# Kernel optimization log

Measured on AMD Instinct MI355X. Metric: run time of the kernel, lower is better.

## Reference

```python
import jax, jax.numpy as jnp
import numpy as np

N_NODES = 2_000_000  # divisible by 5 for the final view(-1, 5)
N_EDGES = 32_000_000


def setup_inputs() -> dict:
    key = jax.random.key(0)
    k_x, k_e, k_w, k_b, k_w1, k_b1, k_w2, k_b2 = jax.random.split(key, 8)
    x = jax.random.normal(k_x, (N_NODES, 1), dtype=jnp.float32)
    edge_index = jax.random.randint(k_e, (2, N_EDGES), 0, N_NODES, dtype=jnp.int64)
    # GCNConv(1, 1): linear weight [in=1, out=1] (no bias in lin), separate bias [1]
    w_conv = jax.random.normal(k_w, (1, 1), dtype=jnp.float32)
    b_conv = jax.random.normal(k_b, (1,), dtype=jnp.float32) * 0.1
    # MLP: Linear(2,4) -> ReLU -> Linear(4,1); weights stored as [in, out]
    w1 = jax.random.normal(k_w1, (2, 4), dtype=jnp.float32) * 0.5
    b1 = jax.random.normal(k_b1, (4,), dtype=jnp.float32) * 0.1
    w2 = jax.random.normal(k_w2, (4, 1), dtype=jnp.float32) * 0.5
    b2 = jax.random.normal(k_b2, (1,), dtype=jnp.float32) * 0.1
    return {"x": x, "edge_index": edge_index, "w_conv": w_conv, "b_conv": b_conv,
            "w1": w1, "b1": b1, "w2": w2, "b2": b2}


def reference(x, edge_index, w_conv, b_conv, w1, b1, w2, b2):
    # GCNConv with normalize=False: no self-loops, no degree norm.
    # h = x @ W; out[dst] = sum over incoming edges of h[src]; out += bias
    src, dst = edge_index[0], edge_index[1]
    h = x @ w_conv                                   # [N, 1]
    agg = jax.ops.segment_sum(h[src], dst, num_segments=N_NODES) + b_conv  # [N, 1]
    # intermediate MLP on cat([x_prev, x_prev], dim=1)
    z = jnp.concatenate([agg, agg], axis=1)          # [N, 2]
    z = jnp.maximum(z @ w1 + b1, 0.0) @ w2 + b2      # [N, 1]
    return z.reshape(-1, 5)[:, 0]                    # [N/5]
```

## Files before the change

kernel.cpp:

```cpp
#include <hip/hip_runtime.h>

#define N_NODES 2000000
#define N_EDGES 32000000
#define N_OUT   400000
#define NBUCKET 256
#define BSZ     1568
#define CAP_BLK 64
#define CHUNK   32768
#define CAP_BKT 28672
#define KSLICE  4

typedef int iv4 __attribute__((ext_vector_type(4)));

__global__ __launch_bounds__(256, 2) void p1_bin(
    const int* __restrict__ src,
    const int* __restrict__ dst,
    const float* __restrict__ x,
    unsigned* __restrict__ cnt,
    float* __restrict__ partials,
    unsigned* __restrict__ payload)
{
    __shared__ unsigned s_cur[NBUCKET];
    __shared__ unsigned s_base[NBUCKET];
    __shared__ unsigned s_stage[NBUCKET][CAP_BLK];

    const int tid = threadIdx.x;
    if (tid < NBUCKET) s_cur[tid] = 0;
    __syncthreads();

    const long long blockStart = (long long)blockIdx.x * CHUNK;
    const int NIT = CHUNK / 1024;

    long long b0 = blockStart + (long long)tid * 4;
    bool valid0 = (b0 < N_EDGES);
    iv4 d4 = valid0 ? *reinterpret_cast<const iv4*>(dst + b0) : (iv4)0;
    iv4 s4 = valid0 ? *reinterpret_cast<const iv4*>(src + b0) : (iv4)0;

    for (int it = 0; it < NIT; ++it) {
        iv4 nd = (iv4)0, ns = (iv4)0;
        bool nvalid = false;
        if (it + 1 < NIT) {
            const long long bn = blockStart + (long long)(it + 1) * 1024 + tid * 4;
            nvalid = (bn < N_EDGES);
            if (nvalid) {
                nd = *reinterpret_cast<const iv4*>(dst + bn);
                ns = *reinterpret_cast<const iv4*>(src + bn);
            }
        }
        if (valid0) {
#pragma unroll
            for (int j = 0; j < 4; ++j) {
                const int d = d4[j];
                if (d % 5 == 0) {
                    const int g = d / 5;
                    const int b = g / BSZ;
                    const unsigned local = (unsigned)(g - b * BSZ);
                    const unsigned p = ((unsigned)s4[j] << 11) | local;
                    const unsigned slot = atomicAdd(&s_cur[b], 1u);
                    if (slot < CAP_BLK) {
                        s_stage[b][slot] = p;
                    } else {
                        const float v = x[s4[j]];
                        atomicAdd(&partials[((size_t)b * (KSLICE + 1) + KSLICE) * BSZ + local], v);
                    }
                }
            }
        }
        d4 = nd; s4 = ns; valid0 = nvalid;
    }
    __syncthreads();

    if (tid < NBUCKET) {
        const unsigned c = min(s_cur[tid], (unsigned)CAP_BLK);
        s_cur[tid] = c;
        s_base[tid] = atomicAdd(&cnt[tid], c);
    }
    __syncthreads();

    const int wave = tid >> 6, lane = tid & 63;
    for (int b = wave; b < NBUCKET; b += 4) {
        const unsigned c = s_cur[b];
        if ((unsigned)lane < c)
            payload[(size_t)b * CAP_BKT + s_base[b] + lane] = s_stage[b][lane];
    }
}

__global__ __launch_bounds__(256) void p2_accum(
    const unsigned* __restrict__ cnt,
    const unsigned* __restrict__ payload,
    const float* __restrict__ x,
    float* __restrict__ partials)
{
    __shared__ float acc[BSZ];
    const int b = blockIdx.x >> 2;
    const int j = blockIdx.x & 3;
    const int tid = threadIdx.x;

    for (int i = tid; i < BSZ; i += 256) acc[i] = 0.0f;
    __syncthreads();

    unsigned n = cnt[b];
    if (n > CAP_BKT) n = CAP_BKT;
    const unsigned beg = (unsigned)(((unsigned long long)n * j) / KSLICE);
    const unsigned end = (unsigned)(((unsigned long long)n * (j + 1)) / KSLICE);
    const unsigned* pb = payload + (size_t)b * CAP_BKT;

    unsigned i0 = beg + tid;
    for (; i0 + 7u * 256u < end; i0 += 8u * 256u) {
        unsigned pv[8]; float vv[8];
#pragma unroll
        for (int u = 0; u < 8; ++u) pv[u] = pb[i0 + u * 256u];
#pragma unroll
        for (int u = 0; u < 8; ++u) vv[u] = x[pv[u] >> 11];
#pragma unroll
        for (int u = 0; u < 8; ++u)
            __hip_atomic_fetch_add(&acc[pv[u] & 2047u], vv[u],
                                   __ATOMIC_RELAXED, __HIP_MEMORY_SCOPE_WORKGROUP);
    }
    for (; i0 < end; i0 += 256u) {
        const unsigned p = pb[i0];
        const float v = x[p >> 11];
        __hip_atomic_fetch_add(&acc[p & 2047u], v,
                               __ATOMIC_RELAXED, __HIP_MEMORY_SCOPE_WORKGROUP);
    }
    __syncthreads();

    float* row = partials + ((size_t)b * (KSLICE + 1) + j) * BSZ;
    for (int i = tid; i < BSZ; i += 256) row[i] = acc[i];
}

__global__ __launch_bounds__(256) void p3_out(
    const float* __restrict__ partials,
    const float* __restrict__ w_conv,
    const float* __restrict__ b_conv,
    const float* __restrict__ w1,
    const float* __restrict__ b1,
    const float* __restrict__ w2,
    const float* __restrict__ b2,
    float* __restrict__ out)
{
    const int i = blockIdx.x * 256 + threadIdx.x;
    if (i >= N_OUT) return;
    const int b = i / BSZ;
    const int local = i - b * BSZ;
    const float* pr = partials + (size_t)b * (KSLICE + 1) * BSZ + local;
    float s = 0.0f;
#pragma unroll
    for (int r = 0; r <= KSLICE; ++r) s += pr[(size_t)r * BSZ];
    const float a = s * w_conv[0] + b_conv[0];
    float rr = b2[0];
#pragma unroll
    for (int jj = 0; jj < 4; ++jj) {
        float t = fmaf(a, w1[jj] + w1[4 + jj], b1[jj]);
        rr = fmaf(fmaxf(t, 0.0f), w2[jj], rr);
    }
    out[i] = rr;
}

__global__ __launch_bounds__(256, 4) void gcn_edge_scatter_dev(
    const int* __restrict__ src,
    const int* __restrict__ dst,
    const float* __restrict__ x,
    float* __restrict__ agg)
{
    const long long base = ((long long)blockIdx.x * blockDim.x + threadIdx.x) * 16;
    if (base >= N_EDGES) return;
    iv4 d4[4], s4[4];
#pragma unroll
    for (int c = 0; c < 4; ++c)
        d4[c] = *(reinterpret_cast<const iv4*>(dst + base) + c);
#pragma unroll
    for (int c = 0; c < 4; ++c)
        s4[c] = *(reinterpret_cast<const iv4*>(src + base) + c);
    int dd[16]; int idx[16]; bool pass[16];
#pragma unroll
    for (int c = 0; c < 4; ++c)
#pragma unroll
        for (int j = 0; j < 4; ++j) {
            const int d = d4[c][j];
            const bool p = (d % 5 == 0);
            dd[c * 4 + j] = d; pass[c * 4 + j] = p;
            idx[c * 4 + j] = p ? s4[c][j] : 0;
        }
    float v[16];
#pragma unroll
    for (int k = 0; k < 16; ++k) v[k] = x[idx[k]];
#pragma unroll
    for (int k = 0; k < 16; ++k)
        if (pass[k]) atomicAdd(&agg[dd[k] / 5], v[k]);
}

__global__ __launch_bounds__(256) void gcn_epilogue_fb(
    const float* __restrict__ agg,
    const float* __restrict__ w_conv, const float* __restrict__ b_conv,
    const float* __restrict__ w1, const float* __restrict__ b1,
    const float* __restrict__ w2, const float* __restrict__ b2,
    float* __restrict__ out)
{
    const int i = blockIdx.x * 256 + threadIdx.x;
    if (i >= N_OUT) return;
    const float a = agg[i] * w_conv[0] + b_conv[0];
    float r = b2[0];
#pragma unroll
    for (int j = 0; j < 4; ++j) {
        float t = fmaf(a, w1[j] + w1[4 + j], b1[j]);
        r = fmaf(fmaxf(t, 0.0f), w2[j], r);
    }
    out[i] = r;
}

extern "C" void kernel_launch(void* const* d_in, const int* in_sizes, int n_in,
                              void* d_out, int out_size, void* d_ws, size_t ws_size,
                              hipStream_t stream) {
    const float* x      = (const float*)d_in[0];
    const int*   ei     = (const int*)  d_in[1];
    const float* w_conv = (const float*)d_in[2];
    const float* b_conv = (const float*)d_in[3];
    const float* w1     = (const float*)d_in[4];
    const float* b1     = (const float*)d_in[5];
    const float* w2     = (const float*)d_in[6];
    const float* b2     = (const float*)d_in[7];
    float* out = (float*)d_out;

    const size_t part_off   = 1024;
    const size_t part_bytes = (size_t)NBUCKET * (KSLICE + 1) * BSZ * sizeof(float);
    const size_t pay_off    = (part_off + part_bytes + 255) & ~(size_t)255;
    const size_t pay_bytes  = (size_t)NBUCKET * CAP_BKT * sizeof(unsigned);
    const size_t need       = pay_off + pay_bytes;

    if (ws_size >= need) {
        unsigned* cnt      = (unsigned*)d_ws;
        float*    partials = (float*)((char*)d_ws + part_off);
        unsigned* payload  = (unsigned*)((char*)d_ws + pay_off);

        (void)hipMemsetAsync(d_ws, 0, pay_off, stream);

        const int grid_p1 = (int)((N_EDGES + CHUNK - 1) / CHUNK);
        p1_bin<<<grid_p1, 256, 0, stream>>>(ei, ei + N_EDGES, x, cnt, partials, payload);
        p2_accum<<<NBUCKET * KSLICE, 256, 0, stream>>>(cnt, payload, x, partials);
        p3_out<<<(N_OUT + 255) / 256, 256, 0, stream>>>(
            partials, w_conv, b_conv, w1, b1, w2, b2, out);
    } else {
        float* agg = (float*)d_ws;
        (void)hipMemsetAsync(agg, 0, (size_t)N_OUT * sizeof(float), stream);
        gcn_edge_scatter_dev<<<(N_EDGES / 16 + 255) / 256, 256, 0, stream>>>(
            ei, ei + N_EDGES, x, agg);
        gcn_epilogue_fb<<<(N_OUT + 255) / 256, 256, 0, stream>>>(
            agg, w_conv, b_conv, w1, b1, w2, b2, out);
    }
}
```

Baseline: 457.0 us.

## Shrink binning chunk, split overflow buffer, vectorize accumulation and raise occupancy

Halves the per-block edge chunk and staging capacity so p1 uses less LDS and can run four blocks per CU, and uses nontemporal loads for the streamed edge arrays. Moves overflow accumulation into its own buffer so only counters and overflow need zeroing, shrinking the memset. Pads bucket counters to separate cache lines, and rewrites the p1 writeback to cover two buckets per wave. p2 now uses 512-thread blocks with 4-wide payload loads. Smaller staging raises the chance of spills into the global atomic overflow path.

```diff
diff --git a/kernel.cpp b/kernel.cpp
--- a/kernel.cpp
+++ b/kernel.cpp
@@ -5,19 +5,21 @@
 #define N_OUT   400000
 #define NBUCKET 256
 #define BSZ     1568
-#define CAP_BLK 64
-#define CHUNK   32768
+#define CAP_BLK 32
+#define CHUNK   16384
 #define CAP_BKT 28672
 #define KSLICE  4
+#define CNT_STRIDE 16
 
 typedef int iv4 __attribute__((ext_vector_type(4)));
-
-__global__ __launch_bounds__(256, 2) void p1_bin(
+typedef unsigned uv4 __attribute__((ext_vector_type(4)));
+
+__global__ __launch_bounds__(256, 4) void p1_bin(
     const int* __restrict__ src,
     const int* __restrict__ dst,
     const float* __restrict__ x,
     unsigned* __restrict__ cnt,
-    float* __restrict__ partials,
+    float* __restrict__ overflow,
     unsigned* __restrict__ payload)
 {
     __shared__ unsigned s_cur[NBUCKET];
@@ -33,8 +35,8 @@
 
     long long b0 = blockStart + (long long)tid * 4;
     bool valid0 = (b0 < N_EDGES);
-    iv4 d4 = valid0 ? *reinterpret_cast<const iv4*>(dst + b0) : (iv4)0;
-    iv4 s4 = valid0 ? *reinterpret_cast<const iv4*>(src + b0) : (iv4)0;
+    iv4 d4 = valid0 ? __builtin_nontemporal_load(reinterpret_cast<const iv4*>(dst + b0)) : (iv4)0;
+    iv4 s4 = valid0 ? __builtin_nontemporal_load(reinterpret_cast<const iv4*>(src + b0)) : (iv4)0;
 
     for (int it = 0; it < NIT; ++it) {
         iv4 nd = (iv4)0, ns = (iv4)0;
@@ -43,25 +45,25 @@
             const long long bn = blockStart + (long long)(it + 1) * 1024 + tid * 4;
             nvalid = (bn < N_EDGES);
             if (nvalid) {
-                nd = *reinterpret_cast<const iv4*>(dst + bn);
-                ns = *reinterpret_cast<const iv4*>(src + bn);
+                nd = __builtin_nontemporal_load(reinterpret_cast<const iv4*>(dst + bn));
+                ns = __builtin_nontemporal_load(reinterpret_cast<const iv4*>(src + bn));
             }
         }
         if (valid0) {
 #pragma unroll
             for (int j = 0; j < 4; ++j) {
-                const int d = d4[j];
-                if (d % 5 == 0) {
-                    const int g = d / 5;
-                    const int b = g / BSZ;
-                    const unsigned local = (unsigned)(g - b * BSZ);
+                const unsigned d = (unsigned)d4[j];
+                if (d % 5u == 0u) {
+                    const unsigned g = d / 5u;
+                    const unsigned b = g / (unsigned)BSZ;
+                    const unsigned local = g - b * (unsigned)BSZ;
                     const unsigned p = ((unsigned)s4[j] << 11) | local;
                     const unsigned slot = atomicAdd(&s_cur[b], 1u);
                     if (slot < CAP_BLK) {
                         s_stage[b][slot] = p;
                     } else {
                         const float v = x[s4[j]];
-                        atomicAdd(&partials[((size_t)b * (KSLICE + 1) + KSLICE) * BSZ + local], v);
+                        atomicAdd(&overflow[(size_t)b * BSZ + local], v);
                     }
                 }
             }
@@ -73,19 +75,22 @@
     if (tid < NBUCKET) {
         const unsigned c = min(s_cur[tid], (unsigned)CAP_BLK);
         s_cur[tid] = c;
-        s_base[tid] = atomicAdd(&cnt[tid], c);
+        s_base[tid] = atomicAdd(&cnt[tid * CNT_STRIDE], c);
     }
     __syncthreads();
 
     const int wave = tid >> 6, lane = tid & 63;
-    for (int b = wave; b < NBUCKET; b += 4) {
+    const int half = lane >> 5, l = lane & 31;
+    for (int i = 0; i < 32; ++i) {
+        const int b = wave * 64 + i * 2 + half;
         const unsigned c = s_cur[b];
-        if ((unsigned)lane < c)
-            payload[(size_t)b * CAP_BKT + s_base[b] + lane] = s_stage[b][lane];
-    }
-}
-
-__global__ __launch_bounds__(256) void p2_accum(
+        const unsigned pos = s_base[b] + (unsigned)l;
+        if ((unsigned)l < c && pos < (unsigned)CAP_BKT)
+            payload[(size_t)b * CAP_BKT + pos] = s_stage[b][l];
+    }
+}
+
+__global__ __launch_bounds__(512, 8) void p2_accum(
     const unsigned* __restrict__ cnt,
     const unsigned* __restrict__ payload,
     const float* __restrict__ x,
@@ -96,41 +101,44 @@
     const int j = blockIdx.x & 3;
     const int tid = threadIdx.x;
 
-    for (int i = tid; i < BSZ; i += 256) acc[i] = 0.0f;
-    __syncthreads();
-
-    unsigned n = cnt[b];
+    for (int i = tid; i < BSZ; i += 512) acc[i] = 0.0f;
+    __syncthreads();
+
+    unsigned n = cnt[b * CNT_STRIDE];
     if (n > CAP_BKT) n = CAP_BKT;
-    const unsigned beg = (unsigned)(((unsigned long long)n * j) / KSLICE);
-    const unsigned end = (unsigned)(((unsigned long long)n * (j + 1)) / KSLICE);
+    unsigned beg = ((unsigned)(((unsigned long long)n * j) >> 2)) & ~3u;
+    unsigned end = (j == KSLICE - 1) ? n
+                 : ((unsigned)(((unsigned long long)n * (j + 1)) >> 2)) & ~3u;
     const unsigned* pb = payload + (size_t)b * CAP_BKT;
 
-    unsigned i0 = beg + tid;
-    for (; i0 + 7u * 256u < end; i0 += 8u * 256u) {
-        unsigned pv[8]; float vv[8];
-#pragma unroll
-        for (int u = 0; u < 8; ++u) pv[u] = pb[i0 + u * 256u];
-#pragma unroll
-        for (int u = 0; u < 8; ++u) vv[u] = x[pv[u] >> 11];
-#pragma unroll
-        for (int u = 0; u < 8; ++u)
+    unsigned base = beg + (unsigned)tid * 4u;
+    for (; base + 3u < end; base += 512u * 4u) {
+        const uv4 pv = *reinterpret_cast<const uv4*>(pb + base);
+        float vv[4];
+#pragma unroll
+        for (int u = 0; u < 4; ++u) vv[u] = x[pv[u] >> 11];
+#pragma unroll
+        for (int u = 0; u < 4; ++u)
             __hip_atomic_fetch_add(&acc[pv[u] & 2047u], vv[u],
                                    __ATOMIC_RELAXED, __HIP_MEMORY_SCOPE_WORKGROUP);
     }
-    for (; i0 < end; i0 += 256u) {
-        const unsigned p = pb[i0];
-        const float v = x[p >> 11];
-        __hip_atomic_fetch_add(&acc[p & 2047u], v,
-                               __ATOMIC_RELAXED, __HIP_MEMORY_SCOPE_WORKGROUP);
-    }
-    __syncthreads();
-
-    float* row = partials + ((size_t)b * (KSLICE + 1) + j) * BSZ;
-    for (int i = tid; i < BSZ; i += 256) row[i] = acc[i];
+    if (base < end) {
+        const unsigned stop = min(end, base + 4u);
+        for (unsigned i = base; i < stop; ++i) {
+            const unsigned p = pb[i];
+            __hip_atomic_fetch_add(&acc[p & 2047u], x[p >> 11],
+                                   __ATOMIC_RELAXED, __HIP_MEMORY_SCOPE_WORKGROUP);
+        }
+    }
+    __syncthreads();
+
+    float* row = partials + ((size_t)b * KSLICE + j) * BSZ;
+    for (int i = tid; i < BSZ; i += 512) row[i] = acc[i];
 }
 
 __global__ __launch_bounds__(256) void p3_out(
     const float* __restrict__ partials,
+    const float* __restrict__ overflow,
     const float* __restrict__ w_conv,
     const float* __restrict__ b_conv,
     const float* __restrict__ w1,
@@ -143,10 +151,10 @@
     if (i >= N_OUT) return;
     const int b = i / BSZ;
     const int local = i - b * BSZ;
-    const float* pr = partials + (size_t)b * (KSLICE + 1) * BSZ + local;
-    float s = 0.0f;
-#pragma unroll
-    for (int r = 0; r <= KSLICE; ++r) s += pr[(size_t)r * BSZ];
+    const float* pr = partials + (size_t)b * KSLICE * BSZ + local;
+    float s = overflow[(size_t)b * BSZ + local];
+#pragma unroll
+    for (int r = 0; r < KSLICE; ++r) s += pr[(size_t)r * BSZ];
     const float a = s * w_conv[0] + b_conv[0];
     float rr = b2[0];
 #pragma unroll
@@ -222,24 +230,28 @@
     const float* b2     = (const float*)d_in[7];
     float* out = (float*)d_out;
 
-    const size_t part_off   = 1024;
-    const size_t part_bytes = (size_t)NBUCKET * (KSLICE + 1) * BSZ * sizeof(float);
-    const size_t pay_off    = (part_off + part_bytes + 255) & ~(size_t)255;
-    const size_t pay_bytes  = (size_t)NBUCKET * CAP_BKT * sizeof(unsigned);
-    const size_t need       = pay_off + pay_bytes;
+    const size_t cnt_bytes = (size_t)NBUCKET * CNT_STRIDE * sizeof(unsigned);
+    const size_t ovf_off   = cnt_bytes;
+    const size_t ovf_bytes = (size_t)NBUCKET * BSZ * sizeof(float);
+    const size_t part_off  = (ovf_off + ovf_bytes + 255) & ~(size_t)255;
+    const size_t part_bytes= (size_t)NBUCKET * KSLICE * BSZ * sizeof(float);
+    const size_t pay_off   = (part_off + part_bytes + 255) & ~(size_t)255;
+    const size_t pay_bytes = (size_t)NBUCKET * CAP_BKT * sizeof(unsigned);
+    const size_t need      = pay_off + pay_bytes;
 
     if (ws_size >= need) {
         unsigned* cnt      = (unsigned*)d_ws;
+        float*    overflow = (float*)((char*)d_ws + ovf_off);
         float*    partials = (float*)((char*)d_ws + part_off);
         unsigned* payload  = (unsigned*)((char*)d_ws + pay_off);
 
-        (void)hipMemsetAsync(d_ws, 0, pay_off, stream);
+        (void)hipMemsetAsync(d_ws, 0, ovf_off + ovf_bytes, stream);
 
         const int grid_p1 = (int)((N_EDGES + CHUNK - 1) / CHUNK);
-        p1_bin<<<grid_p1, 256, 0, stream>>>(ei, ei + N_EDGES, x, cnt, partials, payload);
-        p2_accum<<<NBUCKET * KSLICE, 256, 0, stream>>>(cnt, payload, x, partials);
+        p1_bin<<<grid_p1, 256, 0, stream>>>(ei, ei + N_EDGES, x, cnt, overflow, payload);
+        p2_accum<<<NBUCKET * KSLICE, 512, 0, stream>>>(cnt, payload, x, partials);
         p3_out<<<(N_OUT + 255) / 256, 256, 0, stream>>>(
-            partials, w_conv, b_conv, w1, b1, w2, b2, out);
+            partials, overflow, w_conv, b_conv, w1, b1, w2, b2, out);
     } else {
         float* agg = (float*)d_ws;
         (void)hipMemsetAsync(agg, 0, (size_t)N_OUT * sizeof(float), stream);
```

Result: faster. 445.9 us (-2.4%).
